# Performance work log

Measured on AMD Instinct MI355X. Metric: run time of the kernel, lower is better.

## Reference

```python
import jax, jax.numpy as jnp
import numpy as np

LN_EPS = 1e-5


def _layernorm(x, g, b):
    mu = x.mean(-1, keepdims=True)
    var = x.var(-1, keepdims=True)
    return (x - mu) / jnp.sqrt(var + LN_EPS) * g + b


def _rel_pos_index(p):
    # static numpy computation, identical to the torch buffer
    coords = np.stack(np.meshgrid(np.arange(p), np.arange(p), indexing='ij'))  # (2,p,p)
    flat = coords.reshape(2, -1)  # (2, p*p)
    rel = flat[:, :, None] - flat[:, None, :]  # (2, N, N)
    rel = rel.transpose(1, 2, 0).copy()
    rel[:, :, 0] += p - 1
    rel[:, :, 1] += p - 1
    rel[:, :, 0] *= 2 * p - 1
    return rel.sum(-1)  # (N, N)


def setup_inputs() -> dict:
    key = jax.random.key(0)
    ks = jax.random.split(key, 8)
    B, H, W, C, heads, p = 32, 56, 56, 384, 12, 7
    hid = 4 * C
    s = 0.02
    return {
        'x': jax.random.normal(ks[0], (B, H * W, C), jnp.float32),
        'norm1_g': jnp.ones((C,), jnp.float32),
        'norm1_b': jnp.zeros((C,), jnp.float32),
        'qkv_w': jax.random.normal(ks[1], (3 * C, C), jnp.float32) * s,
        'qkv_b': jnp.zeros((3 * C,), jnp.float32),
        'rpb_table': jax.random.normal(ks[2], ((2 * p - 1) ** 2, heads), jnp.float32) * s,
        'proj_w': jax.random.normal(ks[3], (C, C), jnp.float32) * s,
        'proj_b': jnp.zeros((C,), jnp.float32),
        'norm2_g': jnp.ones((C,), jnp.float32),
        'norm2_b': jnp.zeros((C,), jnp.float32),
        'fc1_w': jax.random.normal(ks[4], (hid, C), jnp.float32) * s,
        'fc1_b': jnp.zeros((hid,), jnp.float32),
        'fc2_w': jax.random.normal(ks[5], (C, hid), jnp.float32) * s,
        'fc2_b': jnp.zeros((C,), jnp.float32),
        'H': H, 'W': W, 'patch_size': p, 'num_heads': heads,
    }


def reference(x, norm1_g, norm1_b, qkv_w, qkv_b, rpb_table, proj_w, proj_b,
              norm2_g, norm2_b, fc1_w, fc1_b, fc2_w, fc2_b,
              H, W, patch_size, num_heads):
    B, L, C = x.shape
    p = patch_size
    N = p * p
    head_dim = C // num_heads
    scale = head_dim ** -0.5

    shortcut = x
    h = _layernorm(x, norm1_g, norm1_b).reshape(B, H, W, C)
    # partition into (B*nWin, N, C); H, W divisible by p so no padding
    h = h.reshape(B, H // p, p, W // p, p, C).transpose(0, 1, 3, 2, 4, 5)
    patches = h.reshape(-1, N, C)
    Bw = patches.shape[0]

    # IPSA attention
    qkv = patches @ qkv_w.T + qkv_b  # (Bw, N, 3C)
    qkv = qkv.reshape(Bw, N, 3, num_heads, head_dim).transpose(2, 0, 3, 1, 4)
    q, k, v = qkv[0] * scale, qkv[1], qkv[2]  # (Bw, h, N, d)
    attn = jnp.einsum('bhnd,bhmd->bhnm', q, k)
    bias = rpb_table[_rel_pos_index(p).reshape(-1)].reshape(N, N, num_heads)
    attn = attn + bias.transpose(2, 0, 1)[None]
    attn = jax.nn.softmax(attn, axis=-1)
    out = jnp.einsum('bhnm,bhmd->bhnd', attn, v).transpose(0, 2, 1, 3).reshape(Bw, N, C)
    out = out @ proj_w.T + proj_b

    # reverse partition
    out = out.reshape(B, H // p, W // p, p, p, C).transpose(0, 1, 3, 2, 4, 5)
    out = out.reshape(B, H * W, C)

    x = shortcut + out
    y = _layernorm(x, norm2_g, norm2_b)
    y = jax.nn.gelu(y @ fc1_w.T + fc1_b, approximate=False)
    y = y @ fc2_w.T + fc2_b
    return x + y
```

## Files before the change

### kernel.cpp

```cpp
#include <hip/hip_runtime.h>
#include <cstdint>
#include <cstddef>

typedef __bf16 bf16;
typedef __bf16 bf16x4 __attribute__((ext_vector_type(4)));
typedef __bf16 bf16x8 __attribute__((ext_vector_type(8)));
typedef float f32x4 __attribute__((ext_vector_type(4)));

static_assert(sizeof(bf16x8) == 16, "bf16x8 must be 16B");

#define NTOK 100352
#define CDIM 384

#define AS1(p) ((const __attribute__((address_space(1))) void*)(p))
#define AS3(p) ((__attribute__((address_space(3))) void*)(p))

__global__ __launch_bounds__(256) void cvt_k(const float* __restrict__ in,
                                             bf16* __restrict__ out, int n)
{
    const int i = (blockIdx.x * 256 + threadIdx.x) * 4;
    if (i < n) {
        const float4 v = *(const float4*)(in + i);
        bf16x4 o;
        o[0] = (bf16)v.x; o[1] = (bf16)v.y; o[2] = (bf16)v.z; o[3] = (bf16)v.w;
        *(bf16x4*)(out + i) = o;
    }
}

__global__ __launch_bounds__(256) void ln32_k(const float* __restrict__ x,
    const float* __restrict__ g, const float* __restrict__ b, bf16* __restrict__ y)
{
    const int wave = threadIdx.x >> 6, lane = threadIdx.x & 63;
    const size_t row = (size_t)blockIdx.x * 4 + wave;
    const float2* xr = (const float2*)(x + row * CDIM);
    float v[6];
    float s = 0.f, s2 = 0.f;
#pragma unroll
    for (int i = 0; i < 3; i++) {
        const float2 t = xr[lane + i * 64];
        v[2 * i] = t.x; v[2 * i + 1] = t.y;
        s += t.x + t.y; s2 += t.x * t.x + t.y * t.y;
    }
#pragma unroll
    for (int off = 32; off > 0; off >>= 1) {
        s  += __shfl_xor(s, off);
        s2 += __shfl_xor(s2, off);
    }
    const float mu   = s * (1.f / CDIM);
    const float rstd = rsqrtf(s2 * (1.f / CDIM) - mu * mu + 1e-5f);
    const float2* gu = (const float2*)g;
    const float2* bu = (const float2*)b;
    uint32_t* yu = (uint32_t*)(y + row * CDIM);
#pragma unroll
    for (int i = 0; i < 3; i++) {
        const float2 gg = gu[lane + i * 64], bb = bu[lane + i * 64];
        const float o0 = (v[2 * i] - mu) * rstd * gg.x + bb.x;
        const float o1 = (v[2 * i + 1] - mu) * rstd * gg.y + bb.y;
        const uint32_t pk = (uint32_t)__builtin_bit_cast(unsigned short, (bf16)o0)
                          | ((uint32_t)__builtin_bit_cast(unsigned short, (bf16)o1) << 16);
        yu[lane + i * 64] = pk;
    }
}

template <int EPI, typename TO>
__global__ __launch_bounds__(256) void gemm_bt(
    const bf16* __restrict__ A, const bf16* __restrict__ Bm,
    const float* __restrict__ bias, const float* __restrict__ res,
    TO* __restrict__ Cc, int N, int K)
{
    __shared__ __align__(16) bf16 lds[2][2][128 * 32];
    const int tid = threadIdx.x;

    const int gx = gridDim.x;
    const int nwg = gx * gridDim.y;
    const int orig = blockIdx.y * gx + blockIdx.x;
    const int q = nwg >> 3, r = nwg & 7;
    const int xcd = orig & 7, lid = orig >> 3;
    const int swz = (xcd < r ? xcd * (q + 1) : r * (q + 1) + (xcd - r) * q) + lid;
    const int m0 = (swz / gx) * 128, n0 = (swz % gx) * 128;

    const int wave = tid >> 6, lane = tid & 63;
    const int wm = (wave >> 1) * 64, wn = (wave & 1) * 64;
    const int lm = lane & 15, lk = (lane >> 4) * 8;

    const int sr = tid >> 2;
    const int sc = (tid & 3) * 8;

    const bf16* Ap0 = A + (size_t)(m0 + sr) * K + sc;
    const bf16* Ap1 = A + (size_t)(m0 + sr + 64) * K + sc;
    const bf16* Bp0 = Bm + (size_t)(n0 + sr) * K + sc;
    const bf16* Bp1 = Bm + (size_t)(n0 + sr + 64) * K + sc;

#define STAGE(buf, koff) do {                                                           \
    __builtin_amdgcn_global_load_lds(AS1(Ap0 + (koff)),                                 \
        AS3(&lds[buf][0][(wave * 16) * 32]), 16, 0, 0);                                 \
    __builtin_amdgcn_global_load_lds(AS1(Ap1 + (koff)),                                 \
        AS3(&lds[buf][0][(64 + wave * 16) * 32]), 16, 0, 0);                            \
    __builtin_amdgcn_global_load_lds(AS1(Bp0 + (koff)),                                 \
        AS3(&lds[buf][1][(wave * 16) * 32]), 16, 0, 0);                                 \
    __builtin_amdgcn_global_load_lds(AS1(Bp1 + (koff)),                                 \
        AS3(&lds[buf][1][(64 + wave * 16) * 32]), 16, 0, 0);                            \
} while (0)

    f32x4 acc[4][4] = {};

    const int nt = K >> 5;
    STAGE(0, 0);
    __syncthreads();
    int cur = 0;
    for (int t = 0; t < nt; ++t) {
        const bool more = (t + 1 < nt);
        if (more) STAGE(cur ^ 1, (t + 1) << 5);
        bf16x8 af[4], bfr[4];
#pragma unroll
        for (int i = 0; i < 4; i++)
            af[i] = *(const bf16x8*)&lds[cur][0][(wm + i * 16 + lm) * 32 + lk];
#pragma unroll
        for (int i = 0; i < 4; i++)
            bfr[i] = *(const bf16x8*)&lds[cur][1][(wn + i * 16 + lm) * 32 + lk];
#pragma unroll
        for (int mi = 0; mi < 4; mi++)
#pragma unroll
            for (int ni = 0; ni < 4; ni++)
                acc[mi][ni] = __builtin_amdgcn_mfma_f32_16x16x32_bf16(
                    af[mi], bfr[ni], acc[mi][ni], 0, 0, 0);
        if (more) { __syncthreads(); cur ^= 1; }
    }
#undef STAGE

    if (EPI == 2) {
        const int rb = m0 + wm + (lane >> 4) * 4;
        const int cb = n0 + wn + lm;
#pragma unroll
        for (int ni = 0; ni < 4; ni++) {
            const int col = cb + ni * 16;
            const float bv = bias[col];
#pragma unroll
            for (int mi = 0; mi < 4; mi++) {
#pragma unroll
                for (int r2 = 0; r2 < 4; r2++) {
                    const int row = rb + mi * 16 + r2;
                    float v = acc[mi][ni][r2] + bv;
                    v += res[(size_t)row * N + col];
                    Cc[(size_t)row * N + col] = (TO)v;
                }
            }
        }
    } else {
        __syncthreads();
        bf16* Ct = (bf16*)lds;
        const int rbl = wm + (lane >> 4) * 4;
        const int cbl = wn + lm;
#pragma unroll
        for (int ni = 0; ni < 4; ni++) {
            const float bv = bias[n0 + cbl + ni * 16];
#pragma unroll
            for (int mi = 0; mi < 4; mi++) {
#pragma unroll
                for (int r2 = 0; r2 < 4; r2++) {
                    float v = acc[mi][ni][r2] + bv;
                    if (EPI == 1) {
                        const float p  = fmaf(v * v, 0.07135481627f, 1.59576912161f);
                        const float u2 = fminf(v * p, 80.f);
                        const float e  = __expf(u2);
                        v = v * e * __builtin_amdgcn_rcpf(1.f + e);
                    }
                    Ct[(rbl + mi * 16 + r2) * 128 + cbl + ni * 16] = (bf16)v;
                }
            }
        }
        __syncthreads();
#pragma unroll
        for (int c2 = 0; c2 < 8; ++c2) {
            const int chunk = tid + (c2 << 8);
            const int row = chunk >> 4, c8 = (chunk & 15) << 3;
            *(bf16x8*)((bf16*)Cc + (size_t)(m0 + row) * N + n0 + c8) =
                *(const bf16x8*)&Ct[row * 128 + c8];
        }
    }
}

__global__ __launch_bounds__(256) void attn_k(const bf16* __restrict__ qkv,
    const float* __restrict__ rpb, bf16* __restrict__ out)
{
    const int hd = blockIdx.x;
    const int w  = blockIdx.y;
    const int bb = w >> 6, win = w & 63, wy = win >> 3, wx = win & 7;
    __shared__ int   toks[49];
    __shared__ float biasS[169];
    __shared__ __align__(16) float ks[49][36];
    __shared__ __align__(16) float vs[49][36];
    __shared__ float S[49][50];
    const int tid = threadIdx.x;
    if (tid < 49)
        toks[tid] = bb * 3136 + (wy * 7 + tid / 7) * 56 + wx * 7 + tid % 7;
    if (tid < 169) biasS[tid] = rpb[tid * 12 + hd];
    __syncthreads();
    for (int t = tid; t < 49 * 4; t += 256) {
        const int r = t >> 2, dc = (t & 3) * 8;
        const bf16* p = qkv + (size_t)toks[r] * 1152 + hd * 32 + dc;
        const bf16x8 kv = *(const bf16x8*)(p + 384);
        const bf16x8 vv = *(const bf16x8*)(p + 768);
#pragma unroll
        for (int e = 0; e < 8; e++) { ks[r][dc + e] = (float)kv[e]; vs[r][dc + e] = (float)vv[e]; }
    }
    __syncthreads();
    const int i = tid >> 2, q4 = tid & 3;
    if (i < 49) {
        float qr[32];
        const bf16* qp = qkv + (size_t)toks[i] * 1152 + hd * 32;
#pragma unroll
        for (int c = 0; c < 4; c++) {
            const bf16x8 qv = *(const bf16x8*)(qp + c * 8);
#pragma unroll
            for (int e = 0; e < 8; e++) qr[c * 8 + e] = (float)qv[e] * 0.1767766952966369f;
        }
        const int iy = i / 7, ix = i % 7;
        for (int j = q4; j < 49; j += 4) {
            float dot = 0.f;
#pragma unroll
            for (int dc = 0; dc < 8; dc++) {
                const float4 kk = *(const float4*)&ks[j][dc * 4];
                dot += qr[dc*4]*kk.x + qr[dc*4+1]*kk.y + qr[dc*4+2]*kk.z + qr[dc*4+3]*kk.w;
            }
            S[i][j] = dot + biasS[(iy - j / 7 + 6) * 13 + (ix - j % 7 + 6)];
        }
    }
    __syncthreads();
    if (tid < 49) {
        float mx = -1e30f;
        for (int j = 0; j < 49; j++) mx = fmaxf(mx, S[tid][j]);
        float sum = 0.f;
        for (int j = 0; j < 49; j++) { const float e = __expf(S[tid][j] - mx); S[tid][j] = e; sum += e; }
        const float inv = 1.f / sum;
        for (int j = 0; j < 49; j++) S[tid][j] *= inv;
    }
    __syncthreads();
    if (i < 49) {
        const int dc = q4 * 8;
        float acc[8] = {};
        for (int j = 0; j < 49; j++) {
            const float p = S[i][j];
            const float4 v0 = *(const float4*)&vs[j][dc];
            const float4 v1 = *(const float4*)&vs[j][dc + 4];
            acc[0] += p * v0.x; acc[1] += p * v0.y; acc[2] += p * v0.z; acc[3] += p * v0.w;
            acc[4] += p * v1.x; acc[5] += p * v1.y; acc[6] += p * v1.z; acc[7] += p * v1.w;
        }
        bf16x8 pk;
#pragma unroll
        for (int e = 0; e < 8; e++) pk[e] = (bf16)acc[e];
        *(bf16x8*)(out + (size_t)toks[i] * CDIM + hd * 32 + dc) = pk;
    }
}

extern "C" void kernel_launch(void* const* d_in, const int* in_sizes, int n_in,
                              void* d_out, int out_size, void* d_ws, size_t ws_size,
                              hipStream_t stream) {
    const float* x      = (const float*)d_in[0];
    const float* n1g    = (const float*)d_in[1];
    const float* n1b    = (const float*)d_in[2];
    const float* qkv_w  = (const float*)d_in[3];
    const float* qkv_b  = (const float*)d_in[4];
    const float* rpb    = (const float*)d_in[5];
    const float* proj_w = (const float*)d_in[6];
    const float* proj_b = (const float*)d_in[7];
    const float* n2g    = (const float*)d_in[8];
    const float* n2b    = (const float*)d_in[9];
    const float* fc1_w  = (const float*)d_in[10];
    const float* fc1_b  = (const float*)d_in[11];
    const float* fc2_w  = (const float*)d_in[12];
    const float* fc2_b  = (const float*)d_in[13];
    float* out = (float*)d_out;

    const size_t wBytes = 3538944;
    int nc = 16;
    for (int c : {1, 2, 4, 8}) {
        if (wBytes + ((size_t)NTOK / c) * 3840 <= ws_size) { nc = c; break; }
    }
    const int rowsC = NTOK / nc;
    const int imgsC = 32 / nc;

    char* ws = (char*)d_ws;
    bf16* wqkv  = (bf16*)ws;
    bf16* wproj = wqkv + 442368;
    bf16* wfc1  = wproj + 147456;
    bf16* wfc2  = wfc1 + 589824;
    bf16* bufH  = (bf16*)(ws + wBytes);
    bf16* bufB  = bufH + (size_t)rowsC * CDIM;
    float* x1   = out;

    cvt_k<<<442368 / 1024, 256, 0, stream>>>(qkv_w, wqkv, 442368);
    cvt_k<<<147456 / 1024, 256, 0, stream>>>(proj_w, wproj, 147456);
    cvt_k<<<589824 / 1024, 256, 0, stream>>>(fc1_w, wfc1, 589824);
    cvt_k<<<589824 / 1024, 256, 0, stream>>>(fc2_w, wfc2, 589824);

    for (int c = 0; c < nc; c++) {
        const size_t ro = (size_t)c * rowsC;
        ln32_k<<<rowsC / 4, 256, 0, stream>>>(x + ro * CDIM, n1g, n1b, bufH);
        gemm_bt<0, bf16><<<dim3(1152 / 128, rowsC / 128), 256, 0, stream>>>(
            bufH, wqkv, qkv_b, nullptr, bufB, 1152, 384);
        attn_k<<<dim3(12, 64 * imgsC), 256, 0, stream>>>(bufB, rpb, bufH);
        gemm_bt<2, float><<<dim3(384 / 128, rowsC / 128), 256, 0, stream>>>(
            bufH, wproj, proj_b, x + ro * CDIM, x1 + ro * CDIM, 384, 384);
    }
    for (int c = 0; c < nc; c++) {
        const size_t ro = (size_t)c * rowsC;
        ln32_k<<<rowsC / 4, 256, 0, stream>>>(x1 + ro * CDIM, n2g, n2b, bufH);
        gemm_bt<1, bf16><<<dim3(1536 / 128, rowsC / 128), 256, 0, stream>>>(
            bufH, wfc1, fc1_b, nullptr, bufB, 1536, 384);
        gemm_bt<2, float><<<dim3(384 / 128, rowsC / 128), 256, 0, stream>>>(
            bufB, wfc2, fc2_b, x1 + ro * CDIM, out + ro * CDIM, 384, 1536);
    }
}
```

Before: 1.231 ms.

## Rewrite window attention with bf16 MFMA, one block per window, precomputed bias

```diff
diff --git a/kernel.cpp b/kernel.cpp
--- a/kernel.cpp
+++ b/kernel.cpp
@@ -25,6 +25,19 @@
         o[0] = (bf16)v.x; o[1] = (bf16)v.y; o[2] = (bf16)v.z; o[3] = (bf16)v.w;
         *(bf16x4*)(out + i) = o;
     }
+}
+
+__global__ __launch_bounds__(256) void bias_k(const float* __restrict__ rpb,
+                                              float* __restrict__ biasE)
+{
+    const int t = blockIdx.x * 256 + threadIdx.x;
+    const int i = t & 63, j = (t >> 6) & 63, hd = t >> 12;
+    float v = -3e38f;
+    if (i < 49 && j < 49) {
+        const int iy = i / 7, ix = i % 7, jy = j / 7, jx = j % 7;
+        v = rpb[((jy - iy + 6) * 13 + (jx - ix + 6)) * 12 + hd];
+    }
+    biasE[t] = v;
 }
 
 __global__ __launch_bounds__(256) void ln32_k(const float* __restrict__ x,
@@ -181,75 +194,133 @@
 }
 
 __global__ __launch_bounds__(256) void attn_k(const bf16* __restrict__ qkv,
-    const float* __restrict__ rpb, bf16* __restrict__ out)
-{
-    const int hd = blockIdx.x;
-    const int w  = blockIdx.y;
+    const float* __restrict__ biasE, bf16* __restrict__ out)
+{
+    const int w  = blockIdx.x;
     const int bb = w >> 6, win = w & 63, wy = win >> 3, wx = win & 7;
-    __shared__ int   toks[49];
-    __shared__ float biasS[169];
-    __shared__ __align__(16) float ks[49][36];
-    __shared__ __align__(16) float vs[49][36];
-    __shared__ float S[49][50];
+    __shared__ int toks[64];
+    __shared__ __align__(16) bf16 VT[4][32 * 64];
+    __shared__ __align__(16) bf16 P[4][64 * 64];
     const int tid = threadIdx.x;
-    if (tid < 49)
-        toks[tid] = bb * 3136 + (wy * 7 + tid / 7) * 56 + wx * 7 + tid % 7;
-    if (tid < 169) biasS[tid] = rpb[tid * 12 + hd];
+    if (tid < 64) {
+        const int t = tid < 49 ? tid : 48;
+        toks[tid] = bb * 3136 + (wy * 7 + t / 7) * 56 + wx * 7 + t % 7;
+    }
     __syncthreads();
-    for (int t = tid; t < 49 * 4; t += 256) {
-        const int r = t >> 2, dc = (t & 3) * 8;
-        const bf16* p = qkv + (size_t)toks[r] * 1152 + hd * 32 + dc;
-        const bf16x8 kv = *(const bf16x8*)(p + 384);
-        const bf16x8 vv = *(const bf16x8*)(p + 768);
-#pragma unroll
-        for (int e = 0; e < 8; e++) { ks[r][dc + e] = (float)kv[e]; vs[r][dc + e] = (float)vv[e]; }
-    }
-    __syncthreads();
-    const int i = tid >> 2, q4 = tid & 3;
-    if (i < 49) {
-        float qr[32];
-        const bf16* qp = qkv + (size_t)toks[i] * 1152 + hd * 32;
-#pragma unroll
-        for (int c = 0; c < 4; c++) {
-            const bf16x8 qv = *(const bf16x8*)(qp + c * 8);
-#pragma unroll
-            for (int e = 0; e < 8; e++) qr[c * 8 + e] = (float)qv[e] * 0.1767766952966369f;
-        }
-        const int iy = i / 7, ix = i % 7;
-        for (int j = q4; j < 49; j += 4) {
-            float dot = 0.f;
-#pragma unroll
-            for (int dc = 0; dc < 8; dc++) {
-                const float4 kk = *(const float4*)&ks[j][dc * 4];
-                dot += qr[dc*4]*kk.x + qr[dc*4+1]*kk.y + qr[dc*4+2]*kk.z + qr[dc*4+3]*kk.w;
-            }
-            S[i][j] = dot + biasS[(iy - j / 7 + 6) * 13 + (ix - j % 7 + 6)];
-        }
-    }
-    __syncthreads();
-    if (tid < 49) {
-        float mx = -1e30f;
-        for (int j = 0; j < 49; j++) mx = fmaxf(mx, S[tid][j]);
-        float sum = 0.f;
-        for (int j = 0; j < 49; j++) { const float e = __expf(S[tid][j] - mx); S[tid][j] = e; sum += e; }
-        const float inv = 1.f / sum;
-        for (int j = 0; j < 49; j++) S[tid][j] *= inv;
-    }
-    __syncthreads();
-    if (i < 49) {
-        const int dc = q4 * 8;
-        float acc[8] = {};
-        for (int j = 0; j < 49; j++) {
-            const float p = S[i][j];
-            const float4 v0 = *(const float4*)&vs[j][dc];
-            const float4 v1 = *(const float4*)&vs[j][dc + 4];
-            acc[0] += p * v0.x; acc[1] += p * v0.y; acc[2] += p * v0.z; acc[3] += p * v0.w;
-            acc[4] += p * v1.x; acc[5] += p * v1.y; acc[6] += p * v1.z; acc[7] += p * v1.w;
-        }
-        bf16x8 pk;
-#pragma unroll
-        for (int e = 0; e < 8; e++) pk[e] = (bf16)acc[e];
-        *(bf16x8*)(out + (size_t)toks[i] * CDIM + hd * 32 + dc) = pk;
+
+    const int wave = tid >> 6, lane = tid & 63;
+    const int g = lane >> 4, lr = lane & 15;
+    char* vt = (char*)VT[wave];
+    char* pb = (char*)P[wave];
+
+    for (int hh = 0; hh < 3; ++hh) {
+        const int hd = wave * 3 + hh;
+#pragma unroll
+        for (int c = 0; c < 4; ++c) {
+            const int idx = c * 64 + lane;
+            const int row = idx >> 2, d0 = (idx & 3) * 8;
+            if (row < 49) {
+                const bf16x8 vv = *(const bf16x8*)(qkv + (size_t)toks[row] * 1152 + 768 + hd * 32 + d0);
+#pragma unroll
+                for (int e = 0; e < 8; ++e) {
+                    const int d = d0 + e;
+                    *(bf16*)(vt + (((d * 64 + row) * 2) ^ ((d & 7) << 4))) = vv[e];
+                }
+            } else {
+#pragma unroll
+                for (int e = 0; e < 8; ++e) {
+                    const int d = d0 + e;
+                    *(bf16*)(vt + (((d * 64 + row) * 2) ^ ((d & 7) << 4))) = (bf16)0.f;
+                }
+            }
+        }
+        bf16x8 kf[4], qf[4];
+#pragma unroll
+        for (int b = 0; b < 4; ++b) {
+            const size_t rk = (size_t)toks[b * 16 + lr] * 1152;
+            kf[b] = *(const bf16x8*)(qkv + rk + 384 + hd * 32 + g * 8);
+            qf[b] = *(const bf16x8*)(qkv + rk +       hd * 32 + g * 8);
+        }
+        f32x4 s[4][4] = {};
+#pragma unroll
+        for (int mi = 0; mi < 4; ++mi)
+#pragma unroll
+            for (int nj = 0; nj < 4; ++nj)
+                s[mi][nj] = __builtin_amdgcn_mfma_f32_16x16x32_bf16(kf[mi], qf[nj], s[mi][nj], 0, 0, 0);
+        const float* bh = biasE + hd * 4096;
+#pragma unroll
+        for (int nj = 0; nj < 4; ++nj) {
+            const int j = nj * 16 + lr;
+            const float* bj = bh + j * 64 + g * 4;
+            float mx = -3e38f;
+#pragma unroll
+            for (int mi = 0; mi < 4; ++mi) {
+                const float4 be = *(const float4*)(bj + mi * 16);
+                const float* bp4 = (const float*)&be;
+#pragma unroll
+                for (int r2 = 0; r2 < 4; ++r2) {
+                    const float v = fmaf(s[mi][nj][r2], 0.1767766952966369f, bp4[r2]);
+                    s[mi][nj][r2] = v;
+                    mx = fmaxf(mx, v);
+                }
+            }
+            mx = fmaxf(mx, __shfl_xor(mx, 16));
+            mx = fmaxf(mx, __shfl_xor(mx, 32));
+            float sm = 0.f;
+#pragma unroll
+            for (int mi = 0; mi < 4; ++mi)
+#pragma unroll
+                for (int r2 = 0; r2 < 4; ++r2) {
+                    const float e = __expf(s[mi][nj][r2] - mx);
+                    s[mi][nj][r2] = e;
+                    sm += e;
+                }
+            sm += __shfl_xor(sm, 16);
+            sm += __shfl_xor(sm, 32);
+            const float inv = __builtin_amdgcn_rcpf(sm);
+#pragma unroll
+            for (int mi = 0; mi < 4; ++mi) {
+                bf16x4 pk;
+#pragma unroll
+                for (int r2 = 0; r2 < 4; ++r2) pk[r2] = (bf16)(s[mi][nj][r2] * inv);
+                const int i0 = mi * 16 + g * 4;
+                *(bf16x4*)(pb + (((j * 64 + i0) * 2) ^ ((j & 7) << 4))) = pk;
+            }
+        }
+        f32x4 o[2][4] = {};
+#pragma unroll
+        for (int kb = 0; kb < 2; ++kb) {
+            bf16x8 av[2], bp[4];
+#pragma unroll
+            for (int db = 0; db < 2; ++db) {
+                const int d = db * 16 + lr;
+                av[db] = *(const bf16x8*)(vt + (((d * 64 + kb * 32 + g * 8) * 2) ^ ((d & 7) << 4)));
+            }
+#pragma unroll
+            for (int jb = 0; jb < 4; ++jb) {
+                const int j = jb * 16 + lr;
+                bp[jb] = *(const bf16x8*)(pb + (((j * 64 + kb * 32 + g * 8) * 2) ^ ((j & 7) << 4)));
+            }
+#pragma unroll
+            for (int db = 0; db < 2; ++db)
+#pragma unroll
+                for (int jb = 0; jb < 4; ++jb)
+                    o[db][jb] = __builtin_amdgcn_mfma_f32_16x16x32_bf16(av[db], bp[jb], o[db][jb], 0, 0, 0);
+        }
+#pragma unroll
+        for (int jb = 0; jb < 4; ++jb) {
+            const int j = jb * 16 + lr;
+            if (j < 49) {
+                bf16* op = out + (size_t)toks[j] * CDIM + hd * 32 + g * 4;
+#pragma unroll
+                for (int db = 0; db < 2; ++db) {
+                    bf16x4 pk;
+#pragma unroll
+                    for (int r2 = 0; r2 < 4; ++r2) pk[r2] = (bf16)o[db][jb][r2];
+                    *(bf16x4*)(op + db * 16) = pk;
+                }
+            }
+        }
     }
 }
 
@@ -272,7 +343,7 @@
     const float* fc2_b  = (const float*)d_in[13];
     float* out = (float*)d_out;
 
-    const size_t wBytes = 3538944;
+    const size_t wBytes = 3538944 + 196608;
     int nc = 16;
     for (int c : {1, 2, 4, 8}) {
         if (wBytes + ((size_t)NTOK / c) * 3840 <= ws_size) { nc = c; break; }
@@ -285,6 +356,7 @@
     bf16* wproj = wqkv + 442368;
     bf16* wfc1  = wproj + 147456;
     bf16* wfc2  = wfc1 + 589824;
+    float* biasE = (float*)(ws + 3538944);
     bf16* bufH  = (bf16*)(ws + wBytes);
     bf16* bufB  = bufH + (size_t)rowsC * CDIM;
     float* x1   = out;
@@ -293,13 +365,14 @@
     cvt_k<<<147456 / 1024, 256, 0, stream>>>(proj_w, wproj, 147456);
     cvt_k<<<589824 / 1024, 256, 0, stream>>>(fc1_w, wfc1, 589824);
     cvt_k<<<589824 / 1024, 256, 0, stream>>>(fc2_w, wfc2, 589824);
+    bias_k<<<192, 256, 0, stream>>>(rpb, biasE);
 
     for (int c = 0; c < nc; c++) {
         const size_t ro = (size_t)c * rowsC;
         ln32_k<<<rowsC / 4, 256, 0, stream>>>(x + ro * CDIM, n1g, n1b, bufH);
         gemm_bt<0, bf16><<<dim3(1152 / 128, rowsC / 128), 256, 0, stream>>>(
             bufH, wqkv, qkv_b, nullptr, bufB, 1152, 384);
-        attn_k<<<dim3(12, 64 * imgsC), 256, 0, stream>>>(bufB, rpb, bufH);
+        attn_k<<<dim3(64 * imgsC), 256, 0, stream>>>(bufB, biasE, bufH);
         gemm_bt<2, float><<<dim3(384 / 128, rowsC / 128), 256, 0, stream>>>(
             bufH, wproj, proj_b, x + ro * CDIM, x1 + ro * CDIM, 384, 384);
     }
```

After: 1.116 ms. 9.3% less time.
